# Kernel optimization log

Measured on AMD Instinct MI355X. Metric: run time of the kernel, lower is better.

## Reference

```python
import jax, jax.numpy as jnp
import numpy as np

SEQ, BATCH, HID, OUT = 2048, 128, 256, 2

def setup_inputs() -> dict:
    key = jax.random.key(0)
    ks = jax.random.split(key, 6)
    return {
        "x": jax.random.normal(ks[0], (SEQ, BATCH), dtype=jnp.float32),
        # torch code draws h inside forward: randn*0.01 + 0.5 -> pass as input for determinism
        "h0": jax.random.normal(ks[1], (BATCH, HID), dtype=jnp.float32) * 0.01 + 0.5,
        "W_ih": jax.random.normal(ks[2], (HID, 1), dtype=jnp.float32) * 0.05 + 0.4,
        "W_hh": jax.random.normal(ks[3], (HID, HID), dtype=jnp.float32) * 0.2,
        "W_hh_bias": jax.random.normal(ks[4], (HID, HID), dtype=jnp.float32) * 0.01 + 0.5,
        "b_h": jnp.zeros((HID,), dtype=jnp.float32),
        "W": jax.random.normal(ks[5], (OUT, HID), dtype=jnp.float32) * 0.1 + 0.5,
        "b": jnp.zeros((OUT,), dtype=jnp.float32),
        "context": 1,
    }

def reference(x, h0, W_ih, W_hh, W_hh_bias, b_h, W, b, context):
    # context is a scalar, so c1 + c2 = (2h-1) @ (W_hh + context*W_hh_bias).T (same math, one GEMM)
    W_eff = W_hh + context * W_hh_bias            # (hid, hid)
    w_in = W_ih[:, 0]                             # input_size == 1 -> (hid,)

    def step(h, x_t):
        # c0: (batch,1)@(1,hid) == outer product of x_t with W_ih column
        pre = x_t[:, None] * w_in[None, :] + (2.0 * h - 1.0) @ W_eff.T + b_h
        h_new = jax.nn.sigmoid(pre)
        return h_new, h_new

    _, hs = jax.lax.scan(step, h0, x)             # hs: (seq, batch, hid)
    out = jnp.transpose(hs, (1, 0, 2))            # (batch, seq, hid)
    y = out @ W.T + b                             # (batch, seq, out)
    return y[:, :, 0], out
```

## Files before the change

kernel.cpp:

```cpp
#include <hip/hip_runtime.h>
#include <math.h>

#define SEQ   2048
#define BATCH 128
#define HID   256
#define NCH   16
#define KCH   16
#define VST   20

template <int CTRL>
__device__ __forceinline__ float dpp_mov(float x) {
    return __int_as_float(__builtin_amdgcn_update_dpp(
        __float_as_int(x), __float_as_int(x), CTRL, 0xF, 0xF, false));
}
__device__ __forceinline__ float swz_xor4(float x) {
    return __int_as_float(__builtin_amdgcn_ds_swizzle(__float_as_int(x), 0x101F));
}

__global__ __launch_bounds__(512) __attribute__((amdgpu_waves_per_eu(2, 2)))
void rnn_scan_kernel(const float* __restrict__ x,
                     const float* __restrict__ h0,
                     const float* __restrict__ W_ih,
                     const float* __restrict__ W_hh,
                     const float* __restrict__ W_hh_b,
                     const float* __restrict__ b_h,
                     const int*   __restrict__ context,
                     float*       __restrict__ out_hs)
{
    const int b   = blockIdx.x;
    const int tid = threadIdx.x;
    const int R   = tid >> 4;
    const int l   = tid & 15;
    const int l7  = tid & 7;
    const int row = 8 * R + l7;

    __shared__ __align__(16) float v_lds[2][NCH * VST];
    __shared__ float x_lds[SEQ];

    for (int t = tid; t < SEQ; t += 512)
        x_lds[t] = x[t * BATCH + b];

    const float ctx = (float)context[0];

    float4 wreg[8][4];
    #pragma unroll
    for (int j = 0; j < 8; ++j) {
        const int rj = 8 * R + (l7 ^ j);
        const float* wp = W_hh   + (size_t)rj * HID + KCH * l;
        const float* bp = W_hh_b + (size_t)rj * HID + KCH * l;
        #pragma unroll
        for (int c = 0; c < 4; ++c) {
            const float4 a = *(const float4*)(wp + 4 * c);
            const float4 d = *(const float4*)(bp + 4 * c);
            wreg[j][c] = make_float4(a.x + ctx * d.x, a.y + ctx * d.y,
                                     a.z + ctx * d.z, a.w + ctx * d.w);
        }
    }

    const float winj = W_ih[row];
    const float bhj  = b_h[row];

    const int voff = VST * (row >> 4) + (row & 15);
    v_lds[0][voff] = 2.f * h0[(size_t)b * HID + row] - 1.f;

    float* outp = out_hs + (size_t)b * SEQ * HID + row;

    const float4* vr0 = (const float4*)(v_lds[0] + VST * l);
    const float4* vr1 = (const float4*)(v_lds[1] + VST * l);

    __syncthreads();

    auto step = [&](int t, const float4* __restrict__ vr, float* __restrict__ vw) {
        float q[8] = {0.f, 0.f, 0.f, 0.f, 0.f, 0.f, 0.f, 0.f};
        #pragma unroll
        for (int c = 0; c < 4; ++c) {
            const float4 v4 = vr[c];
            #pragma unroll
            for (int j = 0; j < 8; ++j) {
                const float4 w = wreg[j][c];
                q[j] += w.x * v4.x;
                q[j] += w.y * v4.y;
                q[j] += w.z * v4.z;
                q[j] += w.w * v4.w;
            }
        }
        #pragma unroll
        for (int j = 0; j < 8; ++j) q[j] += dpp_mov<0x128>(q[j]);
        q[0] += dpp_mov<0xB1>(q[1]);
        q[2] += dpp_mov<0xB1>(q[3]);
        q[4] += dpp_mov<0xB1>(q[5]);
        q[6] += dpp_mov<0xB1>(q[7]);
        q[0] += dpp_mov<0x4E>(q[2]);
        q[4] += dpp_mov<0x4E>(q[6]);
        q[0] += swz_xor4(q[4]);

        const float pre = q[0] + bhj + x_lds[t] * winj;
        const float h = 1.f / (1.f + __expf(-pre));
        vw[voff] = 2.f * h - 1.f;
        if ((tid & 8) == 0)
            outp[(size_t)t * HID] = h;
        __syncthreads();
    };

    for (int t = 0; t < SEQ; t += 2) {
        step(t,     vr0, v_lds[1]);
        step(t + 1, vr1, v_lds[0]);
    }
}

__global__ __launch_bounds__(256, 4)
void head_kernel(const float* __restrict__ hs,
                 const float* __restrict__ W,
                 const float* __restrict__ bias,
                 float*       __restrict__ y)
{
    const int tid  = threadIdx.x;
    const int lane = tid & 63;
    const int sub  = lane & 15;
    const int rsub = lane >> 4;

    float4 w0[4];
    #pragma unroll
    for (int u = 0; u < 4; ++u)
        w0[u] = *(const float4*)(W + 4 * (16 * u + sub));
    const float b0 = bias[0];

    const int gwave = (blockIdx.x * blockDim.x + tid) >> 6;
    const int nw    = (gridDim.x * blockDim.x) >> 6;
    const int nq    = (BATCH * SEQ) >> 2;

    for (int q = gwave; q < nq; q += nw) {
        const int rrow = q * 4 + rsub;
        const float* rp = hs + (size_t)rrow * HID;
        float s = 0.f;
        #pragma unroll
        for (int u = 0; u < 4; ++u) {
            const float4 hv = *(const float4*)(rp + 4 * (16 * u + sub));
            s += hv.x * w0[u].x + hv.y * w0[u].y +
                 hv.z * w0[u].z + hv.w * w0[u].w;
        }
        s += __shfl_xor(s, 1, 64);
        s += __shfl_xor(s, 2, 64);
        s += __shfl_xor(s, 4, 64);
        s += __shfl_xor(s, 8, 64);
        if (sub == 0) y[rrow] = s + b0;
    }
}

extern "C" void kernel_launch(void* const* d_in, const int* in_sizes, int n_in,
                              void* d_out, int out_size, void* d_ws, size_t ws_size,
                              hipStream_t stream) {
    const float* x      = (const float*)d_in[0];
    const float* h0     = (const float*)d_in[1];
    const float* W_ih   = (const float*)d_in[2];
    const float* W_hh   = (const float*)d_in[3];
    const float* W_hh_b = (const float*)d_in[4];
    const float* b_h    = (const float*)d_in[5];
    const float* W      = (const float*)d_in[6];
    const float* bias   = (const float*)d_in[7];
    const int*   ctx    = (const int*)d_in[8];

    float* y  = (float*)d_out;
    float* hs = y + (size_t)BATCH * SEQ;

    rnn_scan_kernel<<<BATCH, 512, 0, stream>>>(x, h0, W_ih, W_hh, W_hh_b,
                                               b_h, ctx, hs);
    head_kernel<<<2048, 256, 0, stream>>>(hs, W, bias, y);
}
```

Measured before the change: 1.444 ms.

## Fuse output head into recurrent scan kernel and lighten per-step barrier

Removes the separate head kernel. Each step now computes partial dot products of h with the output weight row, reduces them with DPP within 16 lanes, and stores them in a small double-buffered LDS array. One wave per step finishes the sum one step later and writes y. The LDS-reading swizzle in the reduction becomes a DPP row shift, and __syncthreads is replaced by an explicit lgkmcnt wait plus s_barrier with sched barriers. This saves the head kernel launch and its re-read of all hidden states, at the cost of a little extra work inside the serial step loop.

```diff
diff --git a/kernel.cpp b/kernel.cpp
--- a/kernel.cpp
+++ b/kernel.cpp
@@ -13,8 +13,12 @@
     return __int_as_float(__builtin_amdgcn_update_dpp(
         __float_as_int(x), __float_as_int(x), CTRL, 0xF, 0xF, false));
 }
-__device__ __forceinline__ float swz_xor4(float x) {
-    return __int_as_float(__builtin_amdgcn_ds_swizzle(__float_as_int(x), 0x101F));
+
+__device__ __forceinline__ void lds_barrier() {
+    asm volatile("s_waitcnt lgkmcnt(0)" ::: "memory");
+    __builtin_amdgcn_sched_barrier(0);
+    __builtin_amdgcn_s_barrier();
+    __builtin_amdgcn_sched_barrier(0);
 }
 
 __global__ __launch_bounds__(512) __attribute__((amdgpu_waves_per_eu(2, 2)))
@@ -25,7 +29,10 @@
                      const float* __restrict__ W_hh_b,
                      const float* __restrict__ b_h,
                      const int*   __restrict__ context,
-                     float*       __restrict__ out_hs)
+                     const float* __restrict__ Wout,
+                     const float* __restrict__ bias,
+                     float*       __restrict__ out_hs,
+                     float*       __restrict__ out_y)
 {
     const int b   = blockIdx.x;
     const int tid = threadIdx.x;
@@ -33,9 +40,11 @@
     const int l   = tid & 15;
     const int l7  = tid & 7;
     const int row = 8 * R + l7;
+    const int w   = tid >> 6;
 
     __shared__ __align__(16) float v_lds[2][NCH * VST];
     __shared__ float x_lds[SEQ];
+    __shared__ __align__(16) float ypart[2][32];
 
     for (int t = tid; t < SEQ; t += 512)
         x_lds[t] = x[t * BATCH + b];
@@ -59,29 +68,45 @@
 
     const float winj = W_ih[row];
     const float bhj  = b_h[row];
+    const float w0   = Wout[row];
+    const float b0   = bias[0];
 
     const int voff = VST * (row >> 4) + (row & 15);
     v_lds[0][voff] = 2.f * h0[(size_t)b * HID + row] - 1.f;
 
     float* outp = out_hs + (size_t)b * SEQ * HID + row;
+    float* yp   = out_y  + (size_t)b * SEQ;
 
     const float4* vr0 = (const float4*)(v_lds[0] + VST * l);
     const float4* vr1 = (const float4*)(v_lds[1] + VST * l);
 
-    __syncthreads();
+    lds_barrier();
 
-    auto step = [&](int t, const float4* __restrict__ vr, float* __restrict__ vw) {
+    auto step = [&](int t, const float4* __restrict__ vr,
+                    float* __restrict__ vw, int pb) {
+        const int prev = t - 1;
+        if (prev >= 0 && w == (prev & 7)) {
+            const float4* pp = (const float4*)(ypart[pb ^ 1]);
+            float s = 0.f;
+            #pragma unroll
+            for (int u = 0; u < 8; ++u) {
+                const float4 a = pp[u];
+                s += (a.x + a.y) + (a.z + a.w);
+            }
+            if ((tid & 63) == 0) yp[prev] = s + b0;
+        }
+
         float q[8] = {0.f, 0.f, 0.f, 0.f, 0.f, 0.f, 0.f, 0.f};
         #pragma unroll
         for (int c = 0; c < 4; ++c) {
             const float4 v4 = vr[c];
             #pragma unroll
             for (int j = 0; j < 8; ++j) {
-                const float4 w = wreg[j][c];
-                q[j] += w.x * v4.x;
-                q[j] += w.y * v4.y;
-                q[j] += w.z * v4.z;
-                q[j] += w.w * v4.w;
+                const float4 wv = wreg[j][c];
+                q[j] += wv.x * v4.x;
+                q[j] += wv.y * v4.y;
+                q[j] += wv.z * v4.z;
+                q[j] += wv.w * v4.w;
             }
         }
         #pragma unroll
@@ -92,58 +117,37 @@
         q[6] += dpp_mov<0xB1>(q[7]);
         q[0] += dpp_mov<0x4E>(q[2]);
         q[4] += dpp_mov<0x4E>(q[6]);
-        q[0] += swz_xor4(q[4]);
+        q[0] += dpp_mov<0x124>(q[4]);
 
         const float pre = q[0] + bhj + x_lds[t] * winj;
         const float h = 1.f / (1.f + __expf(-pre));
         vw[voff] = 2.f * h - 1.f;
         if ((tid & 8) == 0)
             outp[(size_t)t * HID] = h;
-        __syncthreads();
+
+        float p = h * w0;
+        p += dpp_mov<0x124>(p);
+        p += dpp_mov<0x122>(p);
+        p += dpp_mov<0x121>(p);
+        if ((tid & 15) == 0) ypart[pb][tid >> 4] = p;
+
+        lds_barrier();
     };
 
     for (int t = 0; t < SEQ; t += 2) {
-        step(t,     vr0, v_lds[1]);
-        step(t + 1, vr1, v_lds[0]);
+        step(t,     vr0, v_lds[1], 0);
+        step(t + 1, vr1, v_lds[0], 1);
     }
-}
 
-__global__ __launch_bounds__(256, 4)
-void head_kernel(const float* __restrict__ hs,
-                 const float* __restrict__ W,
-                 const float* __restrict__ bias,
-                 float*       __restrict__ y)
-{
-    const int tid  = threadIdx.x;
-    const int lane = tid & 63;
-    const int sub  = lane & 15;
-    const int rsub = lane >> 4;
-
-    float4 w0[4];
-    #pragma unroll
-    for (int u = 0; u < 4; ++u)
-        w0[u] = *(const float4*)(W + 4 * (16 * u + sub));
-    const float b0 = bias[0];
-
-    const int gwave = (blockIdx.x * blockDim.x + tid) >> 6;
-    const int nw    = (gridDim.x * blockDim.x) >> 6;
-    const int nq    = (BATCH * SEQ) >> 2;
-
-    for (int q = gwave; q < nq; q += nw) {
-        const int rrow = q * 4 + rsub;
-        const float* rp = hs + (size_t)rrow * HID;
+    if (w == ((SEQ - 1) & 7)) {
+        const float4* pp = (const float4*)(ypart[1]);
         float s = 0.f;
         #pragma unroll
-        for (int u = 0; u < 4; ++u) {
-            const float4 hv = *(const float4*)(rp + 4 * (16 * u + sub));
-            s += hv.x * w0[u].x + hv.y * w0[u].y +
-                 hv.z * w0[u].z + hv.w * w0[u].w;
+        for (int u = 0; u < 8; ++u) {
+            const float4 a = pp[u];
+            s += (a.x + a.y) + (a.z + a.w);
         }
-        s += __shfl_xor(s, 1, 64);
-        s += __shfl_xor(s, 2, 64);
-        s += __shfl_xor(s, 4, 64);
-        s += __shfl_xor(s, 8, 64);
-        if (sub == 0) y[rrow] = s + b0;
+        if ((tid & 63) == 0) yp[SEQ - 1] = s + b0;
     }
 }
 
@@ -164,6 +168,5 @@
     float* hs = y + (size_t)BATCH * SEQ;
 
     rnn_scan_kernel<<<BATCH, 512, 0, stream>>>(x, h0, W_ih, W_hh, W_hh_b,
-                                               b_h, ctx, hs);
-    head_kernel<<<2048, 256, 0, stream>>>(hs, W, bias, y);
+                                               b_h, ctx, W, bias, hs, y);
 }
```

Result: slower. 2.051 ms (+42.0%).

## Process four batch rows per block to share register-resident weights and barriers

Applied to the files above, without the earlier changes.

Each workgroup now runs four independent batch recurrences, interleaved within every timestep. This reuses the same register-held W_eff tile across four batch rows and takes one barrier per timestep instead of one per batch row. The grid shrinks from 128 to 32 blocks, leaving most CUs idle and roughly quadrupling the serial VALU work per step in each block, in exchange for more independent instructions to hide LDS and reduction latency. The final xor-4 swizzle in the cross-lane reduction is also replaced with a DPP row shift.

```diff
diff --git a/kernel.cpp b/kernel.cpp
--- a/kernel.cpp
+++ b/kernel.cpp
@@ -7,14 +7,12 @@
 #define NCH   16
 #define KCH   16
 #define VST   20
+#define NB    4
 
 template <int CTRL>
 __device__ __forceinline__ float dpp_mov(float x) {
     return __int_as_float(__builtin_amdgcn_update_dpp(
         __float_as_int(x), __float_as_int(x), CTRL, 0xF, 0xF, false));
-}
-__device__ __forceinline__ float swz_xor4(float x) {
-    return __int_as_float(__builtin_amdgcn_ds_swizzle(__float_as_int(x), 0x101F));
 }
 
 __global__ __launch_bounds__(512) __attribute__((amdgpu_waves_per_eu(2, 2)))
@@ -27,18 +25,21 @@
                      const int*   __restrict__ context,
                      float*       __restrict__ out_hs)
 {
-    const int b   = blockIdx.x;
+    const int b0  = blockIdx.x * NB;
     const int tid = threadIdx.x;
     const int R   = tid >> 4;
     const int l   = tid & 15;
     const int l7  = tid & 7;
     const int row = 8 * R + l7;
 
-    __shared__ __align__(16) float v_lds[2][NCH * VST];
-    __shared__ float x_lds[SEQ];
+    __shared__ __align__(16) float v_lds[NB][2][NCH * VST];
+    __shared__ float x_lds[NB][SEQ];
 
-    for (int t = tid; t < SEQ; t += 512)
-        x_lds[t] = x[t * BATCH + b];
+    for (int i = tid; i < NB * SEQ; i += 512) {
+        const int p = i >> 11;
+        const int t = i & (SEQ - 1);
+        x_lds[p][t] = x[t * BATCH + (b0 + p)];
+    }
 
     const float ctx = (float)context[0];
 
@@ -61,16 +62,22 @@
     const float bhj  = b_h[row];
 
     const int voff = VST * (row >> 4) + (row & 15);
-    v_lds[0][voff] = 2.f * h0[(size_t)b * HID + row] - 1.f;
+    #pragma unroll
+    for (int p = 0; p < NB; ++p)
+        v_lds[p][0][voff] = 2.f * h0[(size_t)(b0 + p) * HID + row] - 1.f;
 
-    float* outp = out_hs + (size_t)b * SEQ * HID + row;
-
-    const float4* vr0 = (const float4*)(v_lds[0] + VST * l);
-    const float4* vr1 = (const float4*)(v_lds[1] + VST * l);
+    float* outp0 = out_hs + (size_t)(b0 + 0) * SEQ * HID + row;
+    float* outp1 = out_hs + (size_t)(b0 + 1) * SEQ * HID + row;
+    float* outp2 = out_hs + (size_t)(b0 + 2) * SEQ * HID + row;
+    float* outp3 = out_hs + (size_t)(b0 + 3) * SEQ * HID + row;
 
     __syncthreads();
 
-    auto step = [&](int t, const float4* __restrict__ vr, float* __restrict__ vw) {
+    auto phase = [&](int t, const float* __restrict__ vbr,
+                     float* __restrict__ vbw,
+                     const float* __restrict__ xrow,
+                     float* __restrict__ outp) {
+        const float4* vr = (const float4*)(vbr + VST * l);
         float q[8] = {0.f, 0.f, 0.f, 0.f, 0.f, 0.f, 0.f, 0.f};
         #pragma unroll
         for (int c = 0; c < 4; ++c) {
@@ -92,19 +99,26 @@
         q[6] += dpp_mov<0xB1>(q[7]);
         q[0] += dpp_mov<0x4E>(q[2]);
         q[4] += dpp_mov<0x4E>(q[6]);
-        q[0] += swz_xor4(q[4]);
+        q[0] += dpp_mov<0x124>(q[4]);
 
-        const float pre = q[0] + bhj + x_lds[t] * winj;
+        const float pre = q[0] + bhj + xrow[t] * winj;
         const float h = 1.f / (1.f + __expf(-pre));
-        vw[voff] = 2.f * h - 1.f;
+        vbw[voff] = 2.f * h - 1.f;
         if ((tid & 8) == 0)
             outp[(size_t)t * HID] = h;
-        __syncthreads();
     };
 
     for (int t = 0; t < SEQ; t += 2) {
-        step(t,     vr0, v_lds[1]);
-        step(t + 1, vr1, v_lds[0]);
+        phase(t, v_lds[0][0], v_lds[0][1], x_lds[0], outp0);
+        phase(t, v_lds[1][0], v_lds[1][1], x_lds[1], outp1);
+        phase(t, v_lds[2][0], v_lds[2][1], x_lds[2], outp2);
+        phase(t, v_lds[3][0], v_lds[3][1], x_lds[3], outp3);
+        __syncthreads();
+        phase(t + 1, v_lds[0][1], v_lds[0][0], x_lds[0], outp0);
+        phase(t + 1, v_lds[1][1], v_lds[1][0], x_lds[1], outp1);
+        phase(t + 1, v_lds[2][1], v_lds[2][0], x_lds[2], outp2);
+        phase(t + 1, v_lds[3][1], v_lds[3][0], x_lds[3], outp3);
+        __syncthreads();
     }
 }
 
@@ -163,7 +177,7 @@
     float* y  = (float*)d_out;
     float* hs = y + (size_t)BATCH * SEQ;
 
-    rnn_scan_kernel<<<BATCH, 512, 0, stream>>>(x, h0, W_ih, W_hh, W_hh_b,
-                                               b_h, ctx, hs);
+    rnn_scan_kernel<<<BATCH / NB, 512, 0, stream>>>(x, h0, W_ih, W_hh, W_hh_b,
+                                                    b_h, ctx, hs);
     head_kernel<<<2048, 256, 0, stream>>>(hs, W, bias, y);
 }
```

Result: slower. 5.246 ms (+263.2%).
